# Performance work log

Measured on AMD Instinct MI355X. Metric: run time of the kernel, lower is better.

## Reference

```python
import jax, jax.numpy as jnp
import numpy as np

D_MODEL = 2048
D_INNER = 4096
D_CONV = 4
D_STATE = 16
DT_RANK = 128  # (d_model + 15) // 16
EPS = 1e-5
B_SZ, SEQ = 2, 2048


def _silu(x):
    return x * jax.nn.sigmoid(x)


def setup_inputs() -> dict:
    key = jax.random.key(0)
    ks = jax.random.split(key, 10)
    s = lambda k, shape, sc=0.02: jax.random.normal(k, shape, jnp.float32) * sc
    # S4D-real init for A_log, small negative bias for dt (standard Mamba init)
    A_log = jnp.log(jnp.tile(jnp.arange(1, D_STATE + 1, dtype=jnp.float32), (D_INNER, 1)))
    return {
        "hidden_states": jax.random.normal(ks[0], (B_SZ, SEQ, D_MODEL), jnp.float32),
        "norm_scale": jnp.ones((D_MODEL,), jnp.float32),
        "in_proj_w": s(ks[1], (2 * D_INNER, D_MODEL)),
        "conv_w": s(ks[2], (D_INNER, 1, D_CONV), 0.1),
        "conv_b": s(ks[3], (D_INNER,), 0.1),
        "x_proj_w": s(ks[4], (DT_RANK + 2 * D_STATE, D_INNER)),
        "dt_proj_w": s(ks[5], (D_INNER, DT_RANK), 0.1),
        "dt_proj_b": jnp.full((D_INNER,), -4.0, jnp.float32) + s(ks[6], (D_INNER,), 0.1),
        "out_proj_w": s(ks[7], (D_MODEL, D_INNER)),
        "A_log": A_log,
        "D": jnp.ones((D_INNER,), jnp.float32),
    }


def reference(hidden_states, norm_scale, in_proj_w, conv_w, conv_b, x_proj_w,
              dt_proj_w, dt_proj_b, out_proj_w, A_log, D):
    B, L, _ = hidden_states.shape
    residual = hidden_states
    # RMSNorm
    rms = jnp.sqrt(jnp.mean(hidden_states ** 2, axis=-1, keepdims=True) + EPS)
    xn = hidden_states / rms * norm_scale
    # in_proj -> [B, L, 2*d_inner]; torch code keeps this as projected_states
    xz = jnp.einsum('bld,ed->ble', xn, in_proj_w)
    x_in = xz[..., :D_INNER].transpose(0, 2, 1)  # [B, d_inner, L]
    z = xz[..., D_INNER:]                        # [B, L, d_inner]
    # depthwise causal conv1d (padding d_conv-1, truncated to L) + SiLU
    xc = jax.lax.conv_general_dilated(
        x_in, conv_w, window_strides=(1,), padding=[(D_CONV - 1, 0)],
        feature_group_count=D_INNER)
    xc = _silu(xc + conv_b[None, :, None])       # [B, d_inner, L]
    # x_proj -> dt, B, C
    x_dbl = jnp.einsum('bdl,rd->brl', xc, x_proj_w)  # [B, dt_rank+2*d_state, L]
    dt_low = x_dbl[:, :DT_RANK]
    Bm = x_dbl[:, DT_RANK:DT_RANK + D_STATE]         # [B, d_state, L]
    Cm = x_dbl[:, DT_RANK + D_STATE:]                # [B, d_state, L]
    delta = jax.nn.softplus(
        jnp.einsum('dr,brl->bdl', dt_proj_w, dt_low) + dt_proj_b[None, :, None])
    A = -jnp.exp(A_log)                              # [d_inner, d_state]
    # selective scan: h_t = exp(delta_t * A) * h_{t-1} + delta_t * B_t * u_t
    delta_t = delta.transpose(2, 0, 1)  # [L, B, d_inner]
    u_t = xc.transpose(2, 0, 1)         # [L, B, d_inner]
    B_t = Bm.transpose(2, 0, 1)         # [L, B, d_state]
    C_t = Cm.transpose(2, 0, 1)         # [L, B, d_state]

    def step(h, inp):
        d_, b_, c_, u_ = inp
        dA = jnp.exp(d_[..., None] * A)                      # [B, d_inner, d_state]
        h = h * dA + (d_ * u_)[..., None] * b_[:, None, :]   # [B, d_inner, d_state]
        y = jnp.einsum('bds,bs->bd', h, c_)                  # [B, d_inner]
        return h, y

    h0 = jnp.zeros((B, D_INNER, D_STATE), hidden_states.dtype)
    _, ys = jax.lax.scan(step, h0, (delta_t, B_t, C_t, u_t))  # [L, B, d_inner]
    y = ys.transpose(1, 0, 2) + xc.transpose(0, 2, 1) * D     # [B, L, d_inner]
    y = y * _silu(z)
    out = jnp.einsum('bld,od->blo', y, out_proj_w)            # [B, L, d_model]
    return residual + out, xz
```

## Files before the change

kernel.cpp:

```cpp
#include <hip/hip_runtime.h>
#include <cstdint>
#include <cstddef>

#define DM   2048
#define DI   4096
#define DST  16
#define DTR  128
#define SEQL 2048
#define NTOK 4096
#define XZW  8192
#define NCHAIN 8192
#define CL   32
#define NCH  64

typedef short short8 __attribute__((ext_vector_type(8)));
typedef float f32x4 __attribute__((ext_vector_type(4)));

__device__ __forceinline__ short f2bf(float x) {
  union { float f; uint32_t u; } v; v.f = x;
  uint32_t r = v.u + 0x7fffu + ((v.u >> 16) & 1u);
  return (short)(r >> 16);
}
__device__ __forceinline__ float bf2f(short s) {
  union { uint32_t u; float f; } v; v.u = ((uint32_t)(uint16_t)s) << 16;
  return v.f;
}

__device__ __forceinline__ void stage16(const short* g, short* l) {
#if __has_builtin(__builtin_amdgcn_global_load_lds)
  __builtin_amdgcn_global_load_lds((const __attribute__((address_space(1))) void*)g,
                                   (__attribute__((address_space(3))) void*)l, 16, 0, 0);
#else
  *(short8*)l = *(const short8*)g;
#endif
}

__global__ __launch_bounds__(256) void cvt4_k(const float* __restrict__ in,
                                              short* __restrict__ out, int n4) {
  int i = blockIdx.x * 256 + threadIdx.x;
  if (i >= n4) return;
  float4 v = ((const float4*)in)[i];
  short4 o;
  o.x = f2bf(v.x); o.y = f2bf(v.y); o.z = f2bf(v.z); o.w = f2bf(v.w);
  ((short4*)out)[i] = o;
}

__global__ __launch_bounds__(256) void pad_xproj_k(const float* __restrict__ xp,
                                                   short* __restrict__ out) {
  int i = blockIdx.x * 256 + threadIdx.x;
  if (i >= 256 * 1024) return;
  int r = i >> 10;
  float4 v = make_float4(0.f, 0.f, 0.f, 0.f);
  if (r < 160) v = ((const float4*)xp)[i];
  short4 o;
  o.x = f2bf(v.x); o.y = f2bf(v.y); o.z = f2bf(v.z); o.w = f2bf(v.w);
  ((short4*)out)[i] = o;
}

__global__ __launch_bounds__(256) void rmsnorm_k(const float* __restrict__ hs,
                                                 const float* __restrict__ sc,
                                                 short* __restrict__ xn) {
  const int token = blockIdx.x;
  const int tid = threadIdx.x;
  const float* row = hs + (size_t)token * DM;
  float4 a = ((const float4*)row)[tid];
  float4 b = ((const float4*)row)[tid + 256];
  float ss = a.x*a.x + a.y*a.y + a.z*a.z + a.w*a.w
           + b.x*b.x + b.y*b.y + b.z*b.z + b.w*b.w;
  #pragma unroll
  for (int o = 32; o > 0; o >>= 1) ss += __shfl_xor(ss, o);
  __shared__ float wsum[4];
  if ((tid & 63) == 0) wsum[tid >> 6] = ss;
  __syncthreads();
  float tot = wsum[0] + wsum[1] + wsum[2] + wsum[3];
  float inv = rsqrtf(tot * (1.0f / DM) + 1e-5f);
  float4 s1 = ((const float4*)sc)[tid];
  float4 s2 = ((const float4*)sc)[tid + 256];
  short4 o1, o2;
  o1.x = f2bf(a.x * inv * s1.x); o1.y = f2bf(a.y * inv * s1.y);
  o1.z = f2bf(a.z * inv * s1.z); o1.w = f2bf(a.w * inv * s1.w);
  o2.x = f2bf(b.x * inv * s2.x); o2.y = f2bf(b.y * inv * s2.y);
  o2.z = f2bf(b.z * inv * s2.z); o2.w = f2bf(b.w * inv * s2.w);
  ((short4*)xn)[(size_t)token * (DM / 4) + tid] = o1;
  ((short4*)xn)[(size_t)token * (DM / 4) + tid + 256] = o2;
}

template <int MFR, int EPI, int RBY, int RBX>
__global__ __launch_bounds__(512) void gemm_big(const short* __restrict__ A,
                                                const short* __restrict__ B,
                                                int K, int N, int nbx,
                                                float* __restrict__ out_f,
                                                const float* __restrict__ aux_f) {
  constexpr int BM = MFR * 32;
  constexpr int ABYTES = BM * 128;
  constexpr int BBYTES = 256 * 128;
  constexpr int AINSTR = ABYTES / 8192;
  constexpr int BUF = ABYTES + BBYTES;
  __shared__ char lds[2 * BUF];

  const int tid = threadIdx.x;
  const int lane = tid & 63;
  const int wid = tid >> 6;
  const int wm = wid >> 2;
  const int wn = wid & 3;
  const int lr = lane & 15;
  const int lj = lane >> 4;

  const int xcd = blockIdx.x & 7;
  const int idx = blockIdx.x >> 3;
  const int nrgx = nbx / RBX;
  const int by = (xcd / nrgx) * RBY + idx / RBX;
  const int bx = (xcd % nrgx) * RBX + idx % RBX;
  const size_t m0 = (size_t)by * BM;
  const size_t n0 = (size_t)bx * 256;

  const int NT = K >> 6;

  auto stA = [&](int t, char* buf) {
    const int k0 = t << 6;
    #pragma unroll
    for (int s = 0; s < AINSTR; ++s) {
      const int off = s * 8192 + tid * 16;
      const int r = off >> 7;
      const int j = (off >> 4) & 7;
      stage16(A + (m0 + r) * (size_t)K + k0 + ((j ^ (r & 7)) << 3),
              (short*)(buf + off));
    }
  };
  auto stB = [&](int t, char* buf) {
    const int k0 = t << 6;
    #pragma unroll
    for (int s = 0; s < 4; ++s) {
      const int off = s * 8192 + tid * 16;
      const int r = off >> 7;
      const int j = (off >> 4) & 7;
      stage16(B + (n0 + r) * (size_t)K + k0 + ((j ^ (r & 7)) << 3),
              (short*)(buf + ABYTES + off));
    }
  };

  f32x4 acc[MFR][4] = {};

  stA(0, lds);
  stB(0, lds);

  for (int t = 0; t < NT; ++t) {
    char* cur = lds + (t & 1) * BUF;
    char* nxt = lds + ((t + 1) & 1) * BUF;
    const bool more = (t + 1) < NT;
    if (more) {
      stA(t + 1, nxt);
      stB(t + 1, nxt);
      if constexpr (AINSTR == 4) asm volatile("s_waitcnt vmcnt(8)" ::: "memory");
      else                       asm volatile("s_waitcnt vmcnt(6)" ::: "memory");
    } else {
      asm volatile("s_waitcnt vmcnt(0)" ::: "memory");
    }
    __builtin_amdgcn_s_barrier();
    __builtin_amdgcn_sched_barrier(0);
    short8 av[MFR][2];
    short8 bv[4][2];
    #pragma unroll
    for (int f = 0; f < MFR; ++f) {
      const int arow = wm * (BM / 2) + f * 16 + lr;
      #pragma unroll
      for (int ks = 0; ks < 2; ++ks)
        av[f][ks] = *(const short8*)(cur + arow * 128 +
                      ((((ks << 2) + lj) ^ (arow & 7)) << 4));
    }
    #pragma unroll
    for (int g = 0; g < 4; ++g) {
      const int brow = wn * 64 + g * 16 + lr;
      #pragma unroll
      for (int ks = 0; ks < 2; ++ks)
        bv[g][ks] = *(const short8*)(cur + ABYTES + brow * 128 +
                      ((((ks << 2) + lj) ^ (brow & 7)) << 4));
    }
    __builtin_amdgcn_s_setprio(1);
    #pragma unroll
    for (int ks = 0; ks < 2; ++ks)
      #pragma unroll
      for (int f = 0; f < MFR; ++f)
        #pragma unroll
        for (int g = 0; g < 4; ++g)
          acc[f][g] = __builtin_amdgcn_mfma_f32_16x16x32_bf16(av[f][ks], bv[g][ks], acc[f][g], 0, 0, 0);
    __builtin_amdgcn_s_setprio(0);
    __builtin_amdgcn_s_barrier();
  }

  #pragma unroll
  for (int f = 0; f < MFR; ++f)
    #pragma unroll
    for (int g = 0; g < 4; ++g)
      #pragma unroll
      for (int jj = 0; jj < 4; ++jj) {
        const size_t row = m0 + wm * (BM / 2) + f * 16 + lj * 4 + jj;
        const size_t col = n0 + wn * 64 + g * 16 + lr;
        float v = acc[f][g][jj];
        if constexpr (EPI == 3) v += aux_f[row * (size_t)N + col];
        out_f[row * (size_t)N + col] = v;
      }
}

template <int EPI>
__global__ __launch_bounds__(256) void gemm_nt(const short* __restrict__ A,
                                               const short* __restrict__ B,
                                               int ld, int K, int N,
                                               float* __restrict__ out_f,
                                               const float* __restrict__ aux_f,
                                               short* __restrict__ out_bf) {
  __shared__ short As[128 * 64];
  __shared__ short Bs[128 * 64];
  const int tid = threadIdx.x;
  const int lane = tid & 63;
  const int wid = tid >> 6;
  const int wr = wid >> 1, wc = wid & 1;
  const size_t m0 = (size_t)blockIdx.y * 128;
  const size_t n0 = (size_t)blockIdx.x * 128;
  A += (size_t)blockIdx.z * K;
  B += (size_t)blockIdx.z * K;
  f32x4 acc[4][4] = {};
  for (int k0 = 0; k0 < K; k0 += 64) {
    #pragma unroll
    for (int i = 0; i < 4; ++i) {
      const int off = i * 4096 + tid * 16;
      const int r = off >> 7;
      const int ke = (off & 127) >> 1;
      stage16(A + (m0 + r) * (size_t)ld + k0 + ke, &As[off >> 1]);
      stage16(B + (n0 + r) * (size_t)ld + k0 + ke, &Bs[off >> 1]);
    }
    __syncthreads();
    #pragma unroll
    for (int kk = 0; kk < 64; kk += 32) {
      short8 af[4], bfr[4];
      const int kb = kk + (lane >> 4) * 8;
      const int rr = lane & 15;
      #pragma unroll
      for (int f = 0; f < 4; ++f) {
        af[f]  = *(const short8*)&As[(wr * 64 + f * 16 + rr) * 64 + kb];
        bfr[f] = *(const short8*)&Bs[(wc * 64 + f * 16 + rr) * 64 + kb];
      }
      #pragma unroll
      for (int fm = 0; fm < 4; ++fm)
        #pragma unroll
        for (int fn = 0; fn < 4; ++fn)
          acc[fm][fn] = __builtin_amdgcn_mfma_f32_16x16x32_bf16(af[fm], bfr[fn], acc[fm][fn], 0, 0, 0);
    }
    __syncthreads();
  }
  const int rbase = (lane >> 4) * 4;
  const int cbase = lane & 15;
  #pragma unroll
  for (int fm = 0; fm < 4; ++fm) {
    #pragma unroll
    for (int fn = 0; fn < 4; ++fn) {
      #pragma unroll
      for (int j = 0; j < 4; ++j) {
        const size_t row = m0 + wr * 64 + fm * 16 + rbase + j;
        const size_t col = n0 + wc * 64 + fn * 16 + cbase;
        const float v = acc[fm][fn][j];
        if constexpr (EPI == 2) {
          float x = v + aux_f[col];
          float sp = (x > 20.f) ? x : log1pf(__expf(x));
          out_bf[row * (size_t)N + col] = f2bf(sp);
        } else {
          out_f[((size_t)blockIdx.z * NTOK + row) * (size_t)N + col] = v;
        }
      }
    }
  }
}

__global__ __launch_bounds__(256) void xdbl_epi_k(const float* __restrict__ part,
                                                  short* __restrict__ dtl,
                                                  float* __restrict__ Bc,
                                                  float* __restrict__ Cc) {
  const int row = blockIdx.x;
  const int col = threadIdx.x;
  const size_t i = (size_t)row * 256 + col;
  const float v = part[i] + part[(size_t)NTOK * 256 + i]
                + part[(size_t)2 * NTOK * 256 + i]
                + part[(size_t)3 * NTOK * 256 + i];
  if (col < 128)      dtl[(size_t)row * 128 + col] = f2bf(v);
  else if (col < 144) Bc[(size_t)row * 16 + (col - 128)] = v;
  else if (col < 160) Cc[(size_t)row * 16 + (col - 144)] = v;
}

__global__ __launch_bounds__(256) void conv_silu_k(const float* __restrict__ xz,
                                                   const float* __restrict__ cw,
                                                   const float* __restrict__ cb,
                                                   short* __restrict__ xc) {
  const int d = blockIdx.x * 256 + threadIdx.x;
  const int t0 = blockIdx.y * 8;
  const int l0 = t0 & (SEQL - 1);
  const float4 w = ((const float4*)cw)[d];
  const float bias = cb[d];
  float x0 = (l0 >= 3) ? xz[(size_t)(t0 - 3) * XZW + d] : 0.f;
  float x1 = (l0 >= 2) ? xz[(size_t)(t0 - 2) * XZW + d] : 0.f;
  float x2 = (l0 >= 1) ? xz[(size_t)(t0 - 1) * XZW + d] : 0.f;
  #pragma unroll
  for (int i = 0; i < 8; ++i) {
    const float x3 = xz[(size_t)(t0 + i) * XZW + d];
    const float acc = bias + w.x * x0 + w.y * x1 + w.z * x2 + w.w * x3;
    const float sv = acc / (1.f + __expf(-acc));
    xc[(size_t)(t0 + i) * DI + d] = f2bf(sv);
    x0 = x1; x1 = x2; x2 = x3;
  }
}

__global__ __launch_bounds__(256) void scan1_k(const short* __restrict__ del_bf,
                                               const short* __restrict__ xc,
                                               const float* __restrict__ Bc,
                                               const float* __restrict__ alog,
                                               float* __restrict__ hloc,
                                               float* __restrict__ Ssum) {
  const int t = blockIdx.x * 256 + threadIdx.x;
  const int sub = t & 1;
  const int chain = (t >> 1) & (NCHAIN - 1);
  const int chunk = t >> 14;
  const int b = chain >> 12;
  const int d = chain & 4095;
  float A[8];
  #pragma unroll
  for (int j = 0; j < 8; ++j) A[j] = -__expf(alog[d * 16 + sub * 8 + j]);
  float h[8] = {};
  float S = 0.f;
  size_t token = (size_t)b * SEQL + (size_t)chunk * CL;
  #pragma unroll 2
  for (int l = 0; l < CL; ++l, ++token) {
    const float delta = bf2f(del_bf[token * DI + d]);
    const float u = bf2f(xc[token * DI + d]);
    const float du = delta * u;
    S += delta;
    const float4 B0 = ((const float4*)Bc)[token * 4 + sub * 2];
    const float4 B1 = ((const float4*)Bc)[token * 4 + sub * 2 + 1];
    const float Bv[8] = {B0.x, B0.y, B0.z, B0.w, B1.x, B1.y, B1.z, B1.w};
    #pragma unroll
    for (int j = 0; j < 8; ++j)
      h[j] = h[j] * __expf(delta * A[j]) + du * Bv[j];
  }
  const size_t idx = (size_t)(chunk * NCHAIN + chain) * 4 + sub * 2;
  ((float4*)hloc)[idx]     = make_float4(h[0], h[1], h[2], h[3]);
  ((float4*)hloc)[idx + 1] = make_float4(h[4], h[5], h[6], h[7]);
  if (sub == 0) Ssum[chunk * NCHAIN + chain] = S;
}

__global__ __launch_bounds__(256) void scan2_k(float* __restrict__ hloc,
                                               const float* __restrict__ Ssum,
                                               const float* __restrict__ alog) {
  const int t = blockIdx.x * 256 + threadIdx.x;
  const int q = t & 3;
  const int chain = t >> 2;
  const int d = chain & 4095;
  float A[4];
  #pragma unroll
  for (int j = 0; j < 4; ++j) A[j] = -__expf(alog[d * 16 + q * 4 + j]);
  float4 h = make_float4(0.f, 0.f, 0.f, 0.f);
  for (int c = 0; c < NCH; ++c) {
    const size_t idx = (size_t)(c * NCHAIN + chain) * 4 + q;
    const float S = Ssum[c * NCHAIN + chain];
    const float4 hl = ((const float4*)hloc)[idx];
    ((float4*)hloc)[idx] = h;
    h.x = h.x * __expf(A[0] * S) + hl.x;
    h.y = h.y * __expf(A[1] * S) + hl.y;
    h.z = h.z * __expf(A[2] * S) + hl.z;
    h.w = h.w * __expf(A[3] * S) + hl.w;
  }
}

__global__ __launch_bounds__(256) void scan3_k(const short* __restrict__ del_bf,
                                               const short* __restrict__ xc,
                                               const float* __restrict__ Bc,
                                               const float* __restrict__ Cc,
                                               const float* __restrict__ xzbuf,
                                               const float* __restrict__ alog,
                                               const float* __restrict__ dvec,
                                               const float* __restrict__ hin,
                                               short* __restrict__ y) {
  const int t = blockIdx.x * 256 + threadIdx.x;
  const int sub = t & 1;
  const int chain = (t >> 1) & (NCHAIN - 1);
  const int chunk = t >> 14;
  const int b = chain >> 12;
  const int d = chain & 4095;
  float A[8];
  #pragma unroll
  for (int j = 0; j < 8; ++j) A[j] = -__expf(alog[d * 16 + sub * 8 + j]);
  const float Dd = dvec[d];
  const size_t idx = (size_t)(chunk * NCHAIN + chain) * 4 + sub * 2;
  const float4 h0 = ((const float4*)hin)[idx];
  const float4 h1 = ((const float4*)hin)[idx + 1];
  float h[8] = {h0.x, h0.y, h0.z, h0.w, h1.x, h1.y, h1.z, h1.w};
  size_t token = (size_t)b * SEQL + (size_t)chunk * CL;
  #pragma unroll 2
  for (int l = 0; l < CL; ++l, ++token) {
    const float delta = bf2f(del_bf[token * DI + d]);
    const float u = bf2f(xc[token * DI + d]);
    const float du = delta * u;
    const float4 B0 = ((const float4*)Bc)[token * 4 + sub * 2];
    const float4 B1 = ((const float4*)Bc)[token * 4 + sub * 2 + 1];
    const float4 C0 = ((const float4*)Cc)[token * 4 + sub * 2];
    const float4 C1 = ((const float4*)Cc)[token * 4 + sub * 2 + 1];
    const float Bv[8] = {B0.x, B0.y, B0.z, B0.w, B1.x, B1.y, B1.z, B1.w};
    const float Cv[8] = {C0.x, C0.y, C0.z, C0.w, C1.x, C1.y, C1.z, C1.w};
    float yp = 0.f;
    #pragma unroll
    for (int j = 0; j < 8; ++j) {
      h[j] = h[j] * __expf(delta * A[j]) + du * Bv[j];
      yp += h[j] * Cv[j];
    }
    yp += __shfl_xor(yp, 1);
    if (sub == 0) {
      const float z = xzbuf[token * XZW + DI + d];
      const float sz = z / (1.f + __expf(-z));
      y[token * DI + d] = f2bf((yp + u * Dd) * sz);
    }
  }
}

extern "C" void kernel_launch(void* const* d_in, const int* in_sizes, int n_in,
                              void* d_out, int out_size, void* d_ws, size_t ws_size,
                              hipStream_t stream) {
  const float* hs   = (const float*)d_in[0];
  const float* nsc  = (const float*)d_in[1];
  const float* win  = (const float*)d_in[2];
  const float* cw   = (const float*)d_in[3];
  const float* cb   = (const float*)d_in[4];
  const float* wxp  = (const float*)d_in[5];
  const float* wdt  = (const float*)d_in[6];
  const float* bdt  = (const float*)d_in[7];
  const float* wout = (const float*)d_in[8];
  const float* alog = (const float*)d_in[9];
  const float* dvec = (const float*)d_in[10];

  float* out0 = (float*)d_out;
  float* xz   = out0 + (size_t)NTOK * DM;

  char* w = (char*)d_ws;
  size_t off = 0;
  auto alloc = [&](size_t bytes) {
    char* p = w + off;
    off += (bytes + 255) & ~(size_t)255;
    return p;
  };
  short* xn_bf   = (short*)alloc((size_t)NTOK * DM * 2);
  short* win_bf  = (short*)alloc((size_t)XZW * DM * 2);
  short* wout_bf = (short*)alloc((size_t)DM * DI * 2);
  short* wdt_bf  = (short*)alloc((size_t)DI * DTR * 2);
  short* wxp_bf  = (short*)alloc((size_t)256 * DI * 2);
  short* xc_bf   = (short*)alloc((size_t)NTOK * DI * 2);
  short* dtl_bf  = (short*)alloc((size_t)NTOK * DTR * 2);
  float* Bc      = (float*)alloc((size_t)NTOK * DST * 4);
  float* Cc      = (float*)alloc((size_t)NTOK * DST * 4);
  short* del_bf  = (short*)alloc((size_t)NTOK * DI * 2);
  short* y_bf    = (short*)alloc((size_t)NTOK * DI * 2);

  float* xp_part = (float*)win_bf;
  float* hloc    = (float*)win_bf;
  float* Ssum    = (float*)xn_bf;

  cvt4_k<<<16384, 256, 0, stream>>>(win,  win_bf,  (XZW * DM) / 4);
  cvt4_k<<<8192,  256, 0, stream>>>(wout, wout_bf, (DM * DI) / 4);
  cvt4_k<<<512,   256, 0, stream>>>(wdt,  wdt_bf,  (DI * DTR) / 4);
  pad_xproj_k<<<1024, 256, 0, stream>>>(wxp, wxp_bf);

  rmsnorm_k<<<NTOK, 256, 0, stream>>>(hs, nsc, xn_bf);
  gemm_big<8, 0, 8, 8><<<dim3((XZW / 256) * (NTOK / 256)), 512, 0, stream>>>(
      xn_bf, win_bf, DM, XZW, XZW / 256, xz, nullptr);
  conv_silu_k<<<dim3(DI / 256, NTOK / 8), 256, 0, stream>>>(xz, cw, cb, xc_bf);
  gemm_nt<4><<<dim3(2, NTOK / 128, 4), 256, 0, stream>>>(
      xc_bf, wxp_bf, DI, DI / 4, 256, xp_part, nullptr, nullptr);
  xdbl_epi_k<<<NTOK, 256, 0, stream>>>(xp_part, dtl_bf, Bc, Cc);
  gemm_nt<2><<<dim3(DI / 128, NTOK / 128, 1), 256, 0, stream>>>(
      dtl_bf, wdt_bf, DTR, DTR, DI, nullptr, bdt, del_bf);
  scan1_k<<<(NCHAIN * 2 * NCH) / 256, 256, 0, stream>>>(
      del_bf, xc_bf, Bc, alog, hloc, Ssum);
  scan2_k<<<(NCHAIN * 4) / 256, 256, 0, stream>>>(hloc, Ssum, alog);
  scan3_k<<<(NCHAIN * 2 * NCH) / 256, 256, 0, stream>>>(
      del_bf, xc_bf, Bc, Cc, xz, alog, dvec, hloc, y_bf);
  gemm_big<4, 3, 8, 4><<<dim3((DM / 256) * (NTOK / 128)), 512, 0, stream>>>(
      y_bf, wout_bf, DI, DM, DM / 256, out0, hs);
}
```

Baseline: 573.5 us.

## Split GEMM main loop into four interleaved phases with partial A prefetch

Restructures the gemm_big main loop into four quadrant phases. Each phase interleaves LDS fragment reads, global-to-LDS staging of the next tile, and MFMA batches, separated by barriers, so memory traffic overlaps compute more finely. For the in_proj GEMM (PRE=1), half of the A tile for step t+2 is staged into the current buffer once it has been consumed, deepening the prefetch. This adds more barriers per iteration and fragile vmcnt bookkeeping, and lowers register pressure by holding half the A fragments at a time.

Result: no change. 570.7 us (-0.5%).

```diff
diff --git a/kernel.cpp b/kernel.cpp
--- a/kernel.cpp
+++ b/kernel.cpp
@@ -85,7 +85,10 @@
   ((short4*)xn)[(size_t)token * (DM / 4) + tid + 256] = o2;
 }
 
-template <int MFR, int EPI, int RBY, int RBX>
+#define LGKM_FENCE() do { asm volatile("s_waitcnt lgkmcnt(0)" ::: "memory"); \
+                          __builtin_amdgcn_sched_barrier(0); } while (0)
+
+template <int MFR, int EPI, int RBY, int RBX, int PRE>
 __global__ __launch_bounds__(512) void gemm_big(const short* __restrict__ A,
                                                 const short* __restrict__ B,
                                                 int K, int N, int nbx,
@@ -116,76 +119,105 @@
 
   const int NT = K >> 6;
 
-  auto stA = [&](int t, char* buf) {
+  auto stA1 = [&](int t, char* buf, int s) {
     const int k0 = t << 6;
-    #pragma unroll
-    for (int s = 0; s < AINSTR; ++s) {
-      const int off = s * 8192 + tid * 16;
-      const int r = off >> 7;
-      const int j = (off >> 4) & 7;
-      stage16(A + (m0 + r) * (size_t)K + k0 + ((j ^ (r & 7)) << 3),
-              (short*)(buf + off));
-    }
+    const int off = s * 8192 + tid * 16;
+    const int r = off >> 7;
+    const int j = (off >> 4) & 7;
+    stage16(A + (m0 + r) * (size_t)K + k0 + ((j ^ (r & 7)) << 3),
+            (short*)(buf + off));
   };
-  auto stB = [&](int t, char* buf) {
+  auto stB1 = [&](int t, char* buf, int s) {
     const int k0 = t << 6;
-    #pragma unroll
-    for (int s = 0; s < 4; ++s) {
-      const int off = s * 8192 + tid * 16;
-      const int r = off >> 7;
-      const int j = (off >> 4) & 7;
-      stage16(B + (n0 + r) * (size_t)K + k0 + ((j ^ (r & 7)) << 3),
-              (short*)(buf + ABYTES + off));
-    }
+    const int off = s * 8192 + tid * 16;
+    const int r = off >> 7;
+    const int j = (off >> 4) & 7;
+    stage16(B + (n0 + r) * (size_t)K + k0 + ((j ^ (r & 7)) << 3),
+            (short*)(buf + ABYTES + off));
   };
 
+#define READ_A(dst, fbase)                                                   \
+  _Pragma("unroll")                                                          \
+  for (int f = 0; f < MFR / 2; ++f) {                                        \
+    const int arow = wm * (BM / 2) + ((fbase) + f) * 16 + lr;                \
+    _Pragma("unroll")                                                        \
+    for (int ks = 0; ks < 2; ++ks)                                           \
+      dst[f][ks] = *(const short8*)(cur + arow * 128 +                       \
+                     ((((ks << 2) + lj) ^ (arow & 7)) << 4));                \
+  }
+#define READ_B(dst, gbase)                                                   \
+  _Pragma("unroll")                                                          \
+  for (int g = 0; g < 2; ++g) {                                              \
+    const int brow = wn * 64 + ((gbase) + g) * 16 + lr;                      \
+    _Pragma("unroll")                                                        \
+    for (int ks = 0; ks < 2; ++ks)                                           \
+      dst[g][ks] = *(const short8*)(cur + ABYTES + brow * 128 +              \
+                     ((((ks << 2) + lj) ^ (brow & 7)) << 4));                \
+  }
+#define MFMA_Q(fbase, gbase, bvx)                                            \
+  __builtin_amdgcn_s_setprio(1);                                             \
+  _Pragma("unroll")                                                          \
+  for (int ks = 0; ks < 2; ++ks)                                             \
+    _Pragma("unroll")                                                        \
+    for (int f = 0; f < MFR / 2; ++f)                                        \
+      _Pragma("unroll")                                                      \
+      for (int g = 0; g < 2; ++g)                                            \
+        acc[(fbase) + f][(gbase) + g] = __builtin_amdgcn_mfma_f32_16x16x32_bf16( \
+            av[f][ks], bvx[g][ks], acc[(fbase) + f][(gbase) + g], 0, 0, 0);  \
+  __builtin_amdgcn_s_setprio(0);
+
   f32x4 acc[MFR][4] = {};
 
-  stA(0, lds);
-  stB(0, lds);
+  {
+    #pragma unroll
+    for (int s = 0; s < AINSTR; ++s) stA1(0, lds, s);
+    #pragma unroll
+    for (int s = 0; s < 4; ++s) stB1(0, lds, s);
+    if (PRE && NT > 1) { stA1(1, lds + BUF, 0); stA1(1, lds + BUF, 2); }
+    if (PRE && NT > 1) asm volatile("s_waitcnt vmcnt(2)" ::: "memory");
+    else               asm volatile("s_waitcnt vmcnt(0)" ::: "memory");
+    __builtin_amdgcn_s_barrier();
+    __builtin_amdgcn_sched_barrier(0);
+  }
 
   for (int t = 0; t < NT; ++t) {
     char* cur = lds + (t & 1) * BUF;
     char* nxt = lds + ((t + 1) & 1) * BUF;
-    const bool more = (t + 1) < NT;
-    if (more) {
-      stA(t + 1, nxt);
-      stB(t + 1, nxt);
-      if constexpr (AINSTR == 4) asm volatile("s_waitcnt vmcnt(8)" ::: "memory");
-      else                       asm volatile("s_waitcnt vmcnt(6)" ::: "memory");
-    } else {
-      asm volatile("s_waitcnt vmcnt(0)" ::: "memory");
+    const bool m1 = (t + 1) < NT;
+    const bool m2 = (t + 2) < NT;
+    short8 av[MFR / 2][2], bv0[2][2], bv1[2][2];
+
+    READ_A(av, 0);
+    READ_B(bv0, 0);
+    if (m1) {
+      if constexpr (PRE) { stA1(t + 1, nxt, 1); stA1(t + 1, nxt, 3); }
+      else {
+        #pragma unroll
+        for (int s = 0; s < AINSTR; ++s) stA1(t + 1, nxt, s);
+      }
     }
+    LGKM_FENCE();
+    MFMA_Q(0, 0, bv0);
+    __builtin_amdgcn_s_barrier();
+
+    READ_B(bv1, 2);
+    if (m1) { stB1(t + 1, nxt, 0); stB1(t + 1, nxt, 1); }
+    LGKM_FENCE();
+    MFMA_Q(0, 2, bv1);
+    __builtin_amdgcn_s_barrier();
+
+    READ_A(av, MFR / 2);
+    if (m1) { stB1(t + 1, nxt, 2); stB1(t + 1, nxt, 3); }
+    if (PRE && m2) { stA1(t + 2, cur, 0); stA1(t + 2, cur, 2); }
+    LGKM_FENCE();
+    MFMA_Q(MFR / 2, 2, bv1);
+    __builtin_amdgcn_s_barrier();
+
+    MFMA_Q(MFR / 2, 0, bv0);
+    if (PRE && m2) asm volatile("s_waitcnt vmcnt(2)" ::: "memory");
+    else           asm volatile("s_waitcnt vmcnt(0)" ::: "memory");
     __builtin_amdgcn_s_barrier();
     __builtin_amdgcn_sched_barrier(0);
-    short8 av[MFR][2];
-    short8 bv[4][2];
-    #pragma unroll
-    for (int f = 0; f < MFR; ++f) {
-      const int arow = wm * (BM / 2) + f * 16 + lr;
-      #pragma unroll
-      for (int ks = 0; ks < 2; ++ks)
-        av[f][ks] = *(const short8*)(cur + arow * 128 +
-                      ((((ks << 2) + lj) ^ (arow & 7)) << 4));
-    }
-    #pragma unroll
-    for (int g = 0; g < 4; ++g) {
-      const int brow = wn * 64 + g * 16 + lr;
-      #pragma unroll
-      for (int ks = 0; ks < 2; ++ks)
-        bv[g][ks] = *(const short8*)(cur + ABYTES + brow * 128 +
-                      ((((ks << 2) + lj) ^ (brow & 7)) << 4));
-    }
-    __builtin_amdgcn_s_setprio(1);
-    #pragma unroll
-    for (int ks = 0; ks < 2; ++ks)
-      #pragma unroll
-      for (int f = 0; f < MFR; ++f)
-        #pragma unroll
-        for (int g = 0; g < 4; ++g)
-          acc[f][g] = __builtin_amdgcn_mfma_f32_16x16x32_bf16(av[f][ks], bv[g][ks], acc[f][g], 0, 0, 0);
-    __builtin_amdgcn_s_setprio(0);
-    __builtin_amdgcn_s_barrier();
   }
 
   #pragma unroll
@@ -200,6 +232,9 @@
         if constexpr (EPI == 3) v += aux_f[row * (size_t)N + col];
         out_f[row * (size_t)N + col] = v;
       }
+#undef READ_A
+#undef READ_B
+#undef MFMA_Q
 }
 
 template <int EPI>
@@ -465,7 +500,7 @@
   pad_xproj_k<<<1024, 256, 0, stream>>>(wxp, wxp_bf);
 
   rmsnorm_k<<<NTOK, 256, 0, stream>>>(hs, nsc, xn_bf);
-  gemm_big<8, 0, 8, 8><<<dim3((XZW / 256) * (NTOK / 256)), 512, 0, stream>>>(
+  gemm_big<8, 0, 8, 8, 1><<<dim3((XZW / 256) * (NTOK / 256)), 512, 0, stream>>>(
       xn_bf, win_bf, DM, XZW, XZW / 256, xz, nullptr);
   conv_silu_k<<<dim3(DI / 256, NTOK / 8), 256, 0, stream>>>(xz, cw, cb, xc_bf);
   gemm_nt<4><<<dim3(2, NTOK / 128, 4), 256, 0, stream>>>(
@@ -478,6 +513,6 @@
   scan2_k<<<(NCHAIN * 4) / 256, 256, 0, stream>>>(hloc, Ssum, alog);
   scan3_k<<<(NCHAIN * 2 * NCH) / 256, 256, 0, stream>>>(
       del_bf, xc_bf, Bc, Cc, xz, alog, dvec, hloc, y_bf);
-  gemm_big<4, 3, 8, 4><<<dim3((DM / 256) * (NTOK / 128)), 512, 0, stream>>>(
+  gemm_big<4, 3, 8, 4, 0><<<dim3((DM / 256) * (NTOK / 128)), 512, 0, stream>>>(
       y_bf, wout_bf, DI, DM, DM / 256, out0, hs);
 }
```
